# Kernel optimization log

Measured on AMD Instinct MI355X. Metric: run time of the kernel, lower is better.

## Reference

```python
import jax, jax.numpy as jnp
import numpy as np
import math

B, T, D, H = 2, 2048, 1024, 16
DH = D // H


def setup_inputs() -> dict:
    key = jax.random.key(0)
    k1, k2, k3 = jax.random.split(key, 3)
    scale_in = 1.0 / math.sqrt(D)
    x = jax.random.normal(k1, (B, T, D), dtype=jnp.float32)
    w_qkv = jax.random.normal(k2, (D, 3 * D), dtype=jnp.float32) * scale_in
    b_qkv = jnp.zeros((3 * D,), dtype=jnp.float32)
    w_out = jax.random.normal(k3, (D, D), dtype=jnp.float32) * scale_in
    b_out = jnp.zeros((D,), dtype=jnp.float32)
    return {"x": x, "w_qkv": w_qkv, "b_qkv": b_qkv, "w_out": w_out, "b_out": b_out}


def reference(x, w_qkv, b_qkv, w_out, b_out):
    # Fused QKV projection: [B,T,3D]
    qkv = x @ w_qkv + b_qkv
    q, k, v = jnp.split(qkv, 3, axis=-1)
    # [B,H,T,DH]
    q = q.reshape(B, T, H, DH).transpose(0, 2, 1, 3)
    k = k.reshape(B, T, H, DH).transpose(0, 2, 1, 3)
    v = v.reshape(B, T, H, DH).transpose(0, 2, 1, 3)
    # scores: [B,H,T,T]
    scores = jnp.einsum('bhqd,bhkd->bhqk', q, k) / math.sqrt(DH)
    causal_mask = jnp.tril(jnp.ones((T, T), dtype=bool))
    scores = jnp.where(causal_mask, scores, -1e10)
    attn = jax.nn.softmax(scores, axis=-1)
    out = jnp.einsum('bhqk,bhkd->bhqd', attn, v)
    out = out.transpose(0, 2, 1, 3).reshape(B, T, D)
    return out @ w_out + b_out
```

## Files before the change

### kernel.cpp

```cpp
#include <hip/hip_runtime.h>
#include <hip/hip_bf16.h>
#include <stdint.h>

#define Bsz  2
#define Tseq 2048
#define Dmod 1024
#define Hn   16
#define DHd  64

typedef short bf16x8 __attribute__((ext_vector_type(8)));
typedef float f32x4 __attribute__((ext_vector_type(4)));

__device__ __forceinline__ float bf2f(unsigned short u) {
  union { unsigned int i; float f; } v; v.i = ((unsigned int)u) << 16; return v.f;
}
__device__ __forceinline__ unsigned short f2bf(float f) {
  union { float f; unsigned int i; } v; v.f = f;
  unsigned int r = (v.i + 0x7fffu + ((v.i >> 16) & 1u)) >> 16;
  return (unsigned short)r;
}
__device__ __forceinline__ unsigned int pk_bf16(float a, float b) {
  union { __hip_bfloat162 h; unsigned int u; } u2;
  u2.h = __float22bfloat162_rn(make_float2(a, b));
  return u2.u;
}
__device__ __forceinline__ void gl_lds16(const unsigned short* g, unsigned short* l) {
  __builtin_amdgcn_global_load_lds(
      (const __attribute__((address_space(1))) void*)g,
      (__attribute__((address_space(3))) void*)l, 16, 0, 0);
}

__global__ __launch_bounds__(256) void prep(const float* __restrict__ x,
                                            const float* __restrict__ w_qkv,
                                            const float* __restrict__ w_out,
                                            unsigned short* __restrict__ xb,
                                            unsigned short* __restrict__ wqkvT,
                                            unsigned short* __restrict__ woutT) {
  __shared__ unsigned short tile[64][65];
  const int blk = blockIdx.x;
  if (blk < 2048) {
    int idx = blk * 2048 + threadIdx.x * 8;
    float4 a = *(const float4*)&x[idx];
    float4 b = *(const float4*)&x[idx + 4];
    unsigned short o[8];
    o[0] = f2bf(a.x); o[1] = f2bf(a.y); o[2] = f2bf(a.z); o[3] = f2bf(a.w);
    o[4] = f2bf(b.x); o[5] = f2bf(b.y); o[6] = f2bf(b.z); o[7] = f2bf(b.w);
    *(uint4*)&xb[idx] = *(const uint4*)o;
    return;
  }
  const float* in;
  unsigned short* out;
  int K = 1024, N, k0, n0;
  if (blk < 2048 + 768) {
    int t = blk - 2048;
    in = w_qkv; out = wqkvT; N = 3072;
    n0 = (t % 48) * 64; k0 = (t / 48) * 64;
  } else {
    int t = blk - 2816;
    in = w_out; out = woutT; N = 1024;
    n0 = (t % 16) * 64; k0 = (t / 16) * 64;
  }
  for (int i = threadIdx.x; i < 4096; i += 256) {
    int r = i >> 6, c = i & 63;
    tile[r][c] = f2bf(in[(size_t)(k0 + r) * N + n0 + c]);
  }
  __syncthreads();
  for (int i = threadIdx.x; i < 4096; i += 256) {
    int r = i >> 6, c = i & 63;
    out[(size_t)(n0 + r) * K + k0 + c] = tile[c][r];
  }
}

template<int NT>
__global__ __launch_bounds__(256) void gemm_bt(const unsigned short* __restrict__ A,
                                               const unsigned short* __restrict__ Bt,
                                               const float* __restrict__ bias,
                                               int M, int N, int K, int mode,
                                               float* __restrict__ outF,
                                               unsigned short* __restrict__ out0,
                                               unsigned short* __restrict__ out1,
                                               unsigned short* __restrict__ out2) {
  constexpr int JT = NT / 32;
  constexpr int BP = NT / 32;
  __shared__ unsigned short As[128 * 64];
  __shared__ unsigned short Bs[NT * 64];
  const int tid  = threadIdx.x;
  const int lane = tid & 63;
  const int w    = tid >> 6;
  const int m0   = blockIdx.x * 128;
  const int n0   = blockIdx.y * NT;
  const int wr   = (w >> 1) * 64;
  const int wc   = (w & 1) * (NT / 2);

  f32x4 acc[4][JT];
  for (int i = 0; i < 4; i++)
    for (int j = 0; j < JT; j++)
      for (int v = 0; v < 4; v++) acc[i][j][v] = 0.0f;

  const int l16 = lane & 63 & 15;
  const int g   = lane >> 4;
  const int sw  = l16 & 7;

  const int csw = (((lane & 7) ^ (lane >> 3)) & 7) * 8;
  const unsigned short* ga[4];
  const unsigned short* gb[BP];
  unsigned short* la[4];
  unsigned short* lb[BP];
#pragma unroll
  for (int p = 0; p < 4; p++) {
    int r = 32 * w + 8 * p + (lane >> 3);
    ga[p] = A + (size_t)(m0 + r) * K + csw;
    la[p] = &As[(32 * w + 8 * p) * 64];
  }
#pragma unroll
  for (int p = 0; p < BP; p++) {
    int r = (NT / 4) * w + 8 * p + (lane >> 3);
    gb[p] = Bt + (size_t)(n0 + r) * K + csw;
    lb[p] = &Bs[((NT / 4) * w + 8 * p) * 64];
  }

  for (int kt = 0; kt < K; kt += 64) {
    __syncthreads();
#pragma unroll
    for (int p = 0; p < 4; p++) gl_lds16(ga[p] + kt, la[p]);
#pragma unroll
    for (int p = 0; p < BP; p++) gl_lds16(gb[p] + kt, lb[p]);
    __syncthreads();
#pragma unroll
    for (int ks = 0; ks < 2; ks++) {
      bf16x8 af[4], bf[JT];
#pragma unroll
      for (int i = 0; i < 4; i++)
        af[i] = *(const bf16x8*)&As[(wr + i * 16 + l16) * 64 + (((ks * 4 + g) ^ sw) * 8)];
#pragma unroll
      for (int j = 0; j < JT; j++)
        bf[j] = *(const bf16x8*)&Bs[(wc + j * 16 + l16) * 64 + (((ks * 4 + g) ^ sw) * 8)];
#pragma unroll
      for (int i = 0; i < 4; i++)
#pragma unroll
        for (int j = 0; j < JT; j++)
          acc[i][j] = __builtin_amdgcn_mfma_f32_16x16x32_bf16(af[i], bf[j], acc[i][j], 0, 0, 0);
    }
  }

  const int q4 = g * 4;
#pragma unroll
  for (int i = 0; i < 4; i++)
#pragma unroll
    for (int j = 0; j < JT; j++) {
      const int mbase = m0 + wr + i * 16 + q4;
      const int n = n0 + wc + j * 16 + l16;
      float vals[4];
#pragma unroll
      for (int v = 0; v < 4; v++) vals[v] = acc[i][j][v] + bias[n];
      if (mode == 1) {
#pragma unroll
        for (int v = 0; v < 4; v++)
          outF[(size_t)(mbase + v) * N + n] = vals[v];
      } else {
        const int which = n >> 10;
        const int rem = n & 1023;
        const int h = rem >> 6, dd = rem & 63;
        const int b = mbase >> 11, t = mbase & 2047;
        if (which == 2) {
          uint2 uu;
          uu.x = pk_bf16(vals[0], vals[1]);
          uu.y = pk_bf16(vals[2], vals[3]);
          *(uint2*)&out2[((size_t)((b * Hn + h) * DHd + dd)) * Tseq + t] = uu;
        } else {
          unsigned short* dst = (which == 0) ? out0 : out1;
#pragma unroll
          for (int v = 0; v < 4; v++)
            dst[(size_t)((b * Hn + h) * Tseq + t + v) * DHd + dd] = f2bf(vals[v]);
        }
      }
    }
}

__global__ __launch_bounds__(256, 3) void attn_mfma(const unsigned short* __restrict__ Qb,
                                                    const unsigned short* __restrict__ Kb,
                                                    const unsigned short* __restrict__ Vtg,
                                                    unsigned short* __restrict__ O) {
  __shared__ unsigned short Ks[2][64 * 72];
  __shared__ unsigned short Vs[2][64 * 72];
  __shared__ unsigned short Ps[4][16 * 72];

  const int tid  = threadIdx.x;
  const int lane = tid & 63;
  const int w    = tid >> 6;
  const int g    = lane >> 4;
  const int l16  = lane & 15;
  const int bh   = blockIdx.x;
  const int tile = (int)gridDim.y - 1 - (int)blockIdx.y;
  const int q0w  = tile * 64 + w * 16;

  const unsigned short* Qp = Qb  + (size_t)bh * Tseq * DHd;
  const unsigned short* Kp = Kb  + (size_t)bh * Tseq * DHd;
  const unsigned short* Vp = Vtg + (size_t)bh * DHd * Tseq;

  bf16x8 qf[2];
#pragma unroll
  for (int ks = 0; ks < 2; ks++)
    qf[ks] = *(const bf16x8*)&Qp[(size_t)(q0w + l16) * DHd + ks * 32 + g * 8];

  f32x4 Oacc[4];
#pragma unroll
  for (int dt = 0; dt < 4; dt++)
#pragma unroll
    for (int v = 0; v < 4; v++) Oacc[dt][v] = 0.f;

  float mrow = -1e30f, lrow = 0.f;
  unsigned short* Pw = Ps[w];
  const int srow = tid >> 3;
  const int sg8  = (tid & 7) * 8;

  const unsigned short* Kg0 = Kp + (size_t)srow * DHd + sg8;
  const unsigned short* Kg1 = Kp + (size_t)(srow + 32) * DHd + sg8;
  const unsigned short* Vg0 = Vp + (size_t)srow * Tseq + sg8;
  const unsigned short* Vg1 = Vp + (size_t)(srow + 32) * Tseq + sg8;

  {
    uint4 k0 = *(const uint4*)Kg0;
    uint4 k1 = *(const uint4*)Kg1;
    uint4 v0 = *(const uint4*)Vg0;
    uint4 v1 = *(const uint4*)Vg1;
    *(uint4*)&Ks[0][srow * 72 + sg8]        = k0;
    *(uint4*)&Ks[0][(srow + 32) * 72 + sg8] = k1;
    *(uint4*)&Vs[0][srow * 72 + sg8]        = v0;
    *(uint4*)&Vs[0][(srow + 32) * 72 + sg8] = v1;
  }
  __syncthreads();

  for (int c = 0; c <= tile; c++) {
    const int cur = c & 1, nxt = cur ^ 1;
    const bool pref = (c < tile);
    uint4 pk0, pk1, pv0, pv1;
    if (pref) {
      const size_t ko = (size_t)(c + 1) * 64 * DHd;
      const int    vo = (c + 1) * 64;
      pk0 = *(const uint4*)(Kg0 + ko);
      pk1 = *(const uint4*)(Kg1 + ko);
      pv0 = *(const uint4*)(Vg0 + vo);
      pv1 = *(const uint4*)(Vg1 + vo);
    }

    f32x4 st[4];
#pragma unroll
    for (int mt = 0; mt < 4; mt++)
#pragma unroll
      for (int v = 0; v < 4; v++) st[mt][v] = 0.f;
#pragma unroll
    for (int ks = 0; ks < 2; ks++) {
      bf16x8 kf[4];
#pragma unroll
      for (int mt = 0; mt < 4; mt++)
        kf[mt] = *(const bf16x8*)&Ks[cur][(16 * mt + l16) * 72 + ks * 32 + g * 8];
#pragma unroll
      for (int mt = 0; mt < 4; mt++)
        st[mt] = __builtin_amdgcn_mfma_f32_16x16x32_bf16(kf[mt], qf[ks], st[mt], 0, 0, 0);
    }

    const float SC = 0.1803368801f;
    float mx = -1e30f;
    if (c == tile) {
      const int qg = q0w + l16;
#pragma unroll
      for (int mt = 0; mt < 4; mt++)
#pragma unroll
        for (int v = 0; v < 4; v++) {
          float s = st[mt][v] * SC;
          if ((c * 64 + 16 * mt + 4 * g + v) > qg) s = -1e30f;
          st[mt][v] = s;
          mx = fmaxf(mx, s);
        }
    } else {
#pragma unroll
      for (int mt = 0; mt < 4; mt++)
#pragma unroll
        for (int v = 0; v < 4; v++) {
          float s = st[mt][v] * SC;
          st[mt][v] = s;
          mx = fmaxf(mx, s);
        }
    }
    mx = fmaxf(mx, __shfl_xor(mx, 16));
    mx = fmaxf(mx, __shfl_xor(mx, 32));
    const float mn = fmaxf(mrow, mx);
    const float alpha = __builtin_exp2f(mrow - mn);
    mrow = mn;
    float psum = 0.f;
#pragma unroll
    for (int mt = 0; mt < 4; mt++) {
      float p[4];
#pragma unroll
      for (int v = 0; v < 4; v++) { p[v] = __builtin_exp2f(st[mt][v] - mn); psum += p[v]; }
      uint2 uu;
      uu.x = pk_bf16(p[0], p[1]);
      uu.y = pk_bf16(p[2], p[3]);
      *(uint2*)&Pw[l16 * 72 + 16 * mt + 4 * g] = uu;
    }
    psum += __shfl_xor(psum, 16);
    psum += __shfl_xor(psum, 32);
    lrow = lrow * alpha + psum;

    const float a0 = __shfl(alpha, 4 * g + 0);
    const float a1 = __shfl(alpha, 4 * g + 1);
    const float a2 = __shfl(alpha, 4 * g + 2);
    const float a3 = __shfl(alpha, 4 * g + 3);
#pragma unroll
    for (int dt = 0; dt < 4; dt++) {
      Oacc[dt][0] *= a0;
      Oacc[dt][1] *= a1;
      Oacc[dt][2] *= a2;
      Oacc[dt][3] *= a3;
    }

#pragma unroll
    for (int ks = 0; ks < 2; ks++) {
      bf16x8 pf = *(const bf16x8*)&Pw[l16 * 72 + ks * 32 + g * 8];
      bf16x8 vf[4];
#pragma unroll
      for (int dt = 0; dt < 4; dt++)
        vf[dt] = *(const bf16x8*)&Vs[cur][(16 * dt + l16) * 72 + ks * 32 + g * 8];
#pragma unroll
      for (int dt = 0; dt < 4; dt++)
        Oacc[dt] = __builtin_amdgcn_mfma_f32_16x16x32_bf16(pf, vf[dt], Oacc[dt], 0, 0, 0);
    }

    if (pref) {
      *(uint4*)&Ks[nxt][srow * 72 + sg8]        = pk0;
      *(uint4*)&Ks[nxt][(srow + 32) * 72 + sg8] = pk1;
      *(uint4*)&Vs[nxt][srow * 72 + sg8]        = pv0;
      *(uint4*)&Vs[nxt][(srow + 32) * 72 + sg8] = pv1;
      __syncthreads();
    }
  }

  const float l0 = __shfl(lrow, 4 * g + 0);
  const float l1 = __shfl(lrow, 4 * g + 1);
  const float l2 = __shfl(lrow, 4 * g + 2);
  const float l3 = __shfl(lrow, 4 * g + 3);
  const float i0 = 1.f / l0, i1 = 1.f / l1, i2 = 1.f / l2, i3 = 1.f / l3;
  const int b = bh >> 4, h = bh & 15;
#pragma unroll
  for (int dt = 0; dt < 4; dt++) {
    const int d = h * DHd + 16 * dt + l16;
    const size_t r0 = (size_t)(b * Tseq + q0w + 4 * g) * Dmod + d;
    O[r0]            = f2bf(Oacc[dt][0] * i0);
    O[r0 + Dmod]     = f2bf(Oacc[dt][1] * i1);
    O[r0 + 2 * Dmod] = f2bf(Oacc[dt][2] * i2);
    O[r0 + 3 * Dmod] = f2bf(Oacc[dt][3] * i3);
  }
}

extern "C" void kernel_launch(void* const* d_in, const int* in_sizes, int n_in,
                              void* d_out, int out_size, void* d_ws, size_t ws_size,
                              hipStream_t stream) {
  (void)in_sizes; (void)n_in; (void)out_size; (void)ws_size;
  const float* x     = (const float*)d_in[0];
  const float* w_qkv = (const float*)d_in[1];
  const float* b_qkv = (const float*)d_in[2];
  const float* w_out = (const float*)d_in[3];
  const float* b_out = (const float*)d_in[4];
  float* out = (float*)d_out;

  unsigned short* ws    = (unsigned short*)d_ws;
  unsigned short* xb    = ws;
  unsigned short* wqkvT = xb    + (size_t)4194304;
  unsigned short* woutT = wqkvT + (size_t)3072 * 1024;
  unsigned short* Qb    = woutT + (size_t)1024 * 1024;
  unsigned short* Kb    = Qb + (size_t)4194304;
  unsigned short* Vt    = Kb + (size_t)4194304;
  unsigned short* Ob    = xb;

  prep<<<3072, 256, 0, stream>>>(x, w_qkv, w_out, xb, wqkvT, woutT);
  gemm_bt<128><<<dim3(32, 24), 256, 0, stream>>>(xb, wqkvT, b_qkv, 4096, 3072, 1024, 0,
                                                 nullptr, Qb, Kb, Vt);
  attn_mfma<<<dim3(32, 32), 256, 0, stream>>>(Qb, Kb, Vt, Ob);
  gemm_bt<64><<<dim3(32, 16), 256, 0, stream>>>(Ob, woutT, b_out, 4096, 1024, 1024, 1,
                                                out, nullptr, nullptr, nullptr);
}
```

Measured before the change: 179.5 us.

## Double-buffer GEMM LDS tiles and use direct global-to-LDS loads in attention

The GEMM kernel now keeps two LDS buffers for the A and B tiles. It issues the direct global-to-LDS loads for the next K tile before computing the current one, which cuts one barrier per iteration and overlaps the loads with MFMA work. The attention kernel replaces its register-staged K/V prefetch with the same gl_lds16 direct loads, and swaps the padded 72-stride LDS layout for an XOR-swizzled 64-stride layout. This saves registers and LDS. The cost is doubled GEMM LDS use, which may lower occupancy, and the correctness now depends on the async LDS writes finishing before the next barrier.

```diff
diff --git a/kernel.cpp b/kernel.cpp
--- a/kernel.cpp
+++ b/kernel.cpp
@@ -82,8 +82,8 @@
                                                unsigned short* __restrict__ out2) {
   constexpr int JT = NT / 32;
   constexpr int BP = NT / 32;
-  __shared__ unsigned short As[128 * 64];
-  __shared__ unsigned short Bs[NT * 64];
+  __shared__ unsigned short As[2][128 * 64];
+  __shared__ unsigned short Bs[2][NT * 64];
   const int tid  = threadIdx.x;
   const int lane = tid & 63;
   const int w    = tid >> 6;
@@ -97,50 +97,60 @@
     for (int j = 0; j < JT; j++)
       for (int v = 0; v < 4; v++) acc[i][j][v] = 0.0f;
 
-  const int l16 = lane & 63 & 15;
+  const int l16 = lane & 15;
   const int g   = lane >> 4;
   const int sw  = l16 & 7;
 
   const int csw = (((lane & 7) ^ (lane >> 3)) & 7) * 8;
   const unsigned short* ga[4];
   const unsigned short* gb[BP];
-  unsigned short* la[4];
-  unsigned short* lb[BP];
+  unsigned short* la[2][4];
+  unsigned short* lb[2][BP];
 #pragma unroll
   for (int p = 0; p < 4; p++) {
     int r = 32 * w + 8 * p + (lane >> 3);
     ga[p] = A + (size_t)(m0 + r) * K + csw;
-    la[p] = &As[(32 * w + 8 * p) * 64];
+    la[0][p] = &As[0][(32 * w + 8 * p) * 64];
+    la[1][p] = &As[1][(32 * w + 8 * p) * 64];
   }
 #pragma unroll
   for (int p = 0; p < BP; p++) {
     int r = (NT / 4) * w + 8 * p + (lane >> 3);
     gb[p] = Bt + (size_t)(n0 + r) * K + csw;
-    lb[p] = &Bs[((NT / 4) * w + 8 * p) * 64];
-  }
+    lb[0][p] = &Bs[0][((NT / 4) * w + 8 * p) * 64];
+    lb[1][p] = &Bs[1][((NT / 4) * w + 8 * p) * 64];
+  }
+
+#pragma unroll
+  for (int p = 0; p < 4; p++) gl_lds16(ga[p], la[0][p]);
+#pragma unroll
+  for (int p = 0; p < BP; p++) gl_lds16(gb[p], lb[0][p]);
+  __syncthreads();
 
   for (int kt = 0; kt < K; kt += 64) {
-    __syncthreads();
-#pragma unroll
-    for (int p = 0; p < 4; p++) gl_lds16(ga[p] + kt, la[p]);
-#pragma unroll
-    for (int p = 0; p < BP; p++) gl_lds16(gb[p] + kt, lb[p]);
-    __syncthreads();
+    const int cur = (kt >> 6) & 1, nxt = cur ^ 1;
+    if (kt + 64 < K) {
+#pragma unroll
+      for (int p = 0; p < 4; p++) gl_lds16(ga[p] + kt + 64, la[nxt][p]);
+#pragma unroll
+      for (int p = 0; p < BP; p++) gl_lds16(gb[p] + kt + 64, lb[nxt][p]);
+    }
 #pragma unroll
     for (int ks = 0; ks < 2; ks++) {
       bf16x8 af[4], bf[JT];
 #pragma unroll
       for (int i = 0; i < 4; i++)
-        af[i] = *(const bf16x8*)&As[(wr + i * 16 + l16) * 64 + (((ks * 4 + g) ^ sw) * 8)];
+        af[i] = *(const bf16x8*)&As[cur][(wr + i * 16 + l16) * 64 + (((ks * 4 + g) ^ sw) * 8)];
 #pragma unroll
       for (int j = 0; j < JT; j++)
-        bf[j] = *(const bf16x8*)&Bs[(wc + j * 16 + l16) * 64 + (((ks * 4 + g) ^ sw) * 8)];
+        bf[j] = *(const bf16x8*)&Bs[cur][(wc + j * 16 + l16) * 64 + (((ks * 4 + g) ^ sw) * 8)];
 #pragma unroll
       for (int i = 0; i < 4; i++)
 #pragma unroll
         for (int j = 0; j < JT; j++)
           acc[i][j] = __builtin_amdgcn_mfma_f32_16x16x32_bf16(af[i], bf[j], acc[i][j], 0, 0, 0);
     }
+    __syncthreads();
   }
 
   const int q4 = g * 4;
@@ -181,8 +191,8 @@
                                                     const unsigned short* __restrict__ Kb,
                                                     const unsigned short* __restrict__ Vtg,
                                                     unsigned short* __restrict__ O) {
-  __shared__ unsigned short Ks[2][64 * 72];
-  __shared__ unsigned short Vs[2][64 * 72];
+  __shared__ unsigned short Ks[2][64 * 64];
+  __shared__ unsigned short Vs[2][64 * 64];
   __shared__ unsigned short Ps[4][16 * 72];
 
   const int tid  = threadIdx.x;
@@ -211,37 +221,28 @@
 
   float mrow = -1e30f, lrow = 0.f;
   unsigned short* Pw = Ps[w];
-  const int srow = tid >> 3;
-  const int sg8  = (tid & 7) * 8;
-
-  const unsigned short* Kg0 = Kp + (size_t)srow * DHd + sg8;
-  const unsigned short* Kg1 = Kp + (size_t)(srow + 32) * DHd + sg8;
-  const unsigned short* Vg0 = Vp + (size_t)srow * Tseq + sg8;
-  const unsigned short* Vg1 = Vp + (size_t)(srow + 32) * Tseq + sg8;
-
-  {
-    uint4 k0 = *(const uint4*)Kg0;
-    uint4 k1 = *(const uint4*)Kg1;
-    uint4 v0 = *(const uint4*)Vg0;
-    uint4 v1 = *(const uint4*)Vg1;
-    *(uint4*)&Ks[0][srow * 72 + sg8]        = k0;
-    *(uint4*)&Ks[0][(srow + 32) * 72 + sg8] = k1;
-    *(uint4*)&Vs[0][srow * 72 + sg8]        = v0;
-    *(uint4*)&Vs[0][(srow + 32) * 72 + sg8] = v1;
-  }
+
+  const int csw = (((lane & 7) ^ (lane >> 3)) & 7) * 8;
+  const unsigned short* KgB = Kp + (size_t)(16 * w + (lane >> 3)) * DHd + csw;
+  const unsigned short* VgB = Vp + (size_t)(16 * w + (lane >> 3)) * Tseq + csw;
+  unsigned short* KsW[2] = { &Ks[0][16 * w * 64], &Ks[1][16 * w * 64] };
+  unsigned short* VsW[2] = { &Vs[0][16 * w * 64], &Vs[1][16 * w * 64] };
+
+  gl_lds16(KgB,             KsW[0]);
+  gl_lds16(KgB + 8 * DHd,   KsW[0] + 8 * 64);
+  gl_lds16(VgB,             VsW[0]);
+  gl_lds16(VgB + 8 * Tseq,  VsW[0] + 8 * 64);
   __syncthreads();
 
   for (int c = 0; c <= tile; c++) {
     const int cur = c & 1, nxt = cur ^ 1;
-    const bool pref = (c < tile);
-    uint4 pk0, pk1, pv0, pv1;
-    if (pref) {
+    if (c < tile) {
       const size_t ko = (size_t)(c + 1) * 64 * DHd;
       const int    vo = (c + 1) * 64;
-      pk0 = *(const uint4*)(Kg0 + ko);
-      pk1 = *(const uint4*)(Kg1 + ko);
-      pv0 = *(const uint4*)(Vg0 + vo);
-      pv1 = *(const uint4*)(Vg1 + vo);
+      gl_lds16(KgB + ko,            KsW[nxt]);
+      gl_lds16(KgB + ko + 8 * DHd,  KsW[nxt] + 8 * 64);
+      gl_lds16(VgB + vo,            VsW[nxt]);
+      gl_lds16(VgB + vo + 8 * Tseq, VsW[nxt] + 8 * 64);
     }
 
     f32x4 st[4];
@@ -254,7 +255,7 @@
       bf16x8 kf[4];
 #pragma unroll
       for (int mt = 0; mt < 4; mt++)
-        kf[mt] = *(const bf16x8*)&Ks[cur][(16 * mt + l16) * 72 + ks * 32 + g * 8];
+        kf[mt] = *(const bf16x8*)&Ks[cur][(16 * mt + l16) * 64 + (((ks * 4 + g) ^ (l16 & 7)) * 8)];
 #pragma unroll
       for (int mt = 0; mt < 4; mt++)
         st[mt] = __builtin_amdgcn_mfma_f32_16x16x32_bf16(kf[mt], qf[ks], st[mt], 0, 0, 0);
@@ -321,19 +322,13 @@
       bf16x8 vf[4];
 #pragma unroll
       for (int dt = 0; dt < 4; dt++)
-        vf[dt] = *(const bf16x8*)&Vs[cur][(16 * dt + l16) * 72 + ks * 32 + g * 8];
+        vf[dt] = *(const bf16x8*)&Vs[cur][(16 * dt + l16) * 64 + (((ks * 4 + g) ^ (l16 & 7)) * 8)];
 #pragma unroll
       for (int dt = 0; dt < 4; dt++)
         Oacc[dt] = __builtin_amdgcn_mfma_f32_16x16x32_bf16(pf, vf[dt], Oacc[dt], 0, 0, 0);
     }
 
-    if (pref) {
-      *(uint4*)&Ks[nxt][srow * 72 + sg8]        = pk0;
-      *(uint4*)&Ks[nxt][(srow + 32) * 72 + sg8] = pk1;
-      *(uint4*)&Vs[nxt][srow * 72 + sg8]        = pv0;
-      *(uint4*)&Vs[nxt][(srow + 32) * 72 + sg8] = pv1;
-      __syncthreads();
-    }
+    __syncthreads();
   }
 
   const float l0 = __shfl(lrow, 4 * g + 0);
```

Result: no change. 179.9 us (+0.3%).
